# Optimization experiments

Hardware: AMD Instinct MI355X
Metric: run time of the kernel (lower is better)

The kernel has to match this reference:

```python
import jax, jax.numpy as jnp
import numpy as np

H = 8
D_MODEL = 512
D_K = D_MODEL // H


def setup_inputs() -> dict:
    key = jax.random.key(0)
    ks = jax.random.split(key, 12)
    B, S = 4, 2048
    scale = 1.0 / np.sqrt(D_MODEL)
    inp = {
        "query": jax.random.normal(ks[0], (B, S, D_MODEL), jnp.float32),
        "key": jax.random.normal(ks[1], (B, S, D_MODEL), jnp.float32),
        "value": jax.random.normal(ks[2], (B, S, D_MODEL), jnp.float32),
        "mask": jnp.ones((B, 1, S), jnp.int32),
        "Wq": jax.random.normal(ks[3], (D_MODEL, D_MODEL), jnp.float32) * scale,
        "bq": jax.random.normal(ks[4], (D_MODEL,), jnp.float32) * 0.01,
        "Wk": jax.random.normal(ks[5], (D_MODEL, D_MODEL), jnp.float32) * scale,
        "bk": jax.random.normal(ks[6], (D_MODEL,), jnp.float32) * 0.01,
        "Wv": jax.random.normal(ks[7], (D_MODEL, D_MODEL), jnp.float32) * scale,
        "bv": jax.random.normal(ks[8], (D_MODEL,), jnp.float32) * 0.01,
        "Wo": jax.random.normal(ks[9], (D_MODEL, D_MODEL), jnp.float32) * scale,
        "bo": jax.random.normal(ks[10], (D_MODEL,), jnp.float32) * 0.01,
    }
    return inp


def reference(query, key, value, mask, Wq, bq, Wk, bk, Wv, bv, Wo, bo):
    B, S, _ = query.shape

    def proj(x, W, b):
        # [B,S,D] -> [B,H,S,d_k]
        y = jnp.einsum('bsd,ed->bse', x, W) + b  # torch Linear: x @ W.T + b
        return y.reshape(B, S, H, D_K).transpose(0, 2, 1, 3)

    q = proj(query, Wq, bq)
    k = proj(key, Wk, bk)
    v = proj(value, Wv, bv)

    scores = jnp.einsum('bhqd,bhkd->bhqk', q, k) / jnp.sqrt(jnp.float32(D_K))
    m = mask[:, None, :, :]  # [B,1,1,S]
    scores = jnp.where(m == 0, jnp.float32(-1e9), scores)
    p_attn = jax.nn.softmax(scores, axis=-1)  # dropout is identity in eval
    x = jnp.einsum('bhqk,bhkd->bhqd', p_attn, v)
    x = x.transpose(0, 2, 1, 3).reshape(B, S, D_MODEL)
    return jnp.einsum('bsd,ed->bse', x, Wo) + bo
```

## Files before the change

### kernel.cpp

```cpp
#include <hip/hip_runtime.h>
#include <hip/hip_bf16.h>

#define H 8
#define DMODEL 512
#define DK 64
#define BATCH 4
#define SEQ 2048
#define M_TOTAL (BATCH*SEQ)

typedef short bf16x8 __attribute__((ext_vector_type(8)));
typedef float f32x4 __attribute__((ext_vector_type(4)));
typedef float f32x16 __attribute__((ext_vector_type(16)));

__device__ __forceinline__ unsigned short f2bf(float f) {
    unsigned int u = __builtin_bit_cast(unsigned int, f);
    u += 0x7FFFu + ((u >> 16) & 1u);
    return (unsigned short)(u >> 16);
}

__device__ __forceinline__ unsigned int pack_bf2(float a, float b) {
    unsigned int r;
    asm("v_cvt_pk_bf16_f32 %0, %1, %2" : "=v"(r) : "v"(a), "v"(b));
    return r;
}

__device__ __forceinline__ float exp2_fast(float x) {
    float r;
    asm("v_exp_f32 %0, %1" : "=v"(r) : "v"(x));
    return r;
}

__device__ __forceinline__ f32x16 zero16() {
    f32x16 z;
    #pragma unroll
    for (int i = 0; i < 16; i++) z[i] = 0.f;
    return z;
}

__global__ __launch_bounds__(256) void gemm_qkv(
    const float* __restrict__ query, const float* __restrict__ key_,
    const float* __restrict__ value,
    const float* __restrict__ Wq, const float* __restrict__ bq,
    const float* __restrict__ Wk, const float* __restrict__ bk,
    const float* __restrict__ Wv, const float* __restrict__ bv,
    unsigned short* __restrict__ Qh, unsigned short* __restrict__ Kh,
    unsigned short* __restrict__ Vt)
{
    const int z = blockIdx.z;
    const float* A    = (z == 0) ? query : (z == 1) ? key_ : value;
    const float* W    = (z == 0) ? Wq : (z == 1) ? Wk : Wv;
    const float* bias = (z == 0) ? bq : (z == 1) ? bk : bv;
    unsigned short* out = (z == 0) ? Qh : (z == 1) ? Kh : Vt;

    const int m0 = blockIdx.x * 128;
    const int n0 = blockIdx.y * 64;
    const int tid = threadIdx.x;
    const int lane = tid & 63;
    const int w = tid >> 6;
    const int g = lane >> 4, qi = lane & 15;
    const int wm = w >> 1, wn = w & 1;

    __shared__ unsigned short Alds[128 * 40];
    __shared__ unsigned short Blds[64 * 40];

    f32x4 acc[4][2];
    #pragma unroll
    for (int i = 0; i < 4; i++)
        #pragma unroll
        for (int j = 0; j < 2; j++) acc[i][j] = f32x4{0.f, 0.f, 0.f, 0.f};

    float4 aA[4], bA[2], aB[4], bB[2];

    auto ld = [&](float4 (&ar)[4], float4 (&br)[2], int k0) {
        #pragma unroll
        for (int i = 0; i < 4; i++) { int idx = tid + i * 256;
            ar[i] = *(const float4*)(A + (size_t)(m0 + (idx >> 3)) * 512 + k0 + (idx & 7) * 4); }
        #pragma unroll
        for (int i = 0; i < 2; i++) { int idx = tid + i * 256;
            br[i] = *(const float4*)(W + (size_t)(n0 + (idx >> 3)) * 512 + k0 + (idx & 7) * 4); }
    };
    auto st = [&](float4 (&ar)[4], float4 (&br)[2]) {
        #pragma unroll
        for (int i = 0; i < 4; i++) { int idx = tid + i * 256;
            uint2 p; p.x = pack_bf2(ar[i].x, ar[i].y); p.y = pack_bf2(ar[i].z, ar[i].w);
            *(uint2*)(Alds + (idx >> 3) * 40 + (idx & 7) * 4) = p; }
        #pragma unroll
        for (int i = 0; i < 2; i++) { int idx = tid + i * 256;
            uint2 p; p.x = pack_bf2(br[i].x, br[i].y); p.y = pack_bf2(br[i].z, br[i].w);
            *(uint2*)(Blds + (idx >> 3) * 40 + (idx & 7) * 4) = p; }
    };
    auto tile = [&]() {
        bf16x8 af[4], bf[2];
        #pragma unroll
        for (int mt = 0; mt < 4; mt++)
            af[mt] = *(const bf16x8*)(Alds + (wm * 64 + mt * 16 + qi) * 40 + g * 8);
        #pragma unroll
        for (int nt = 0; nt < 2; nt++)
            bf[nt] = *(const bf16x8*)(Blds + (wn * 32 + nt * 16 + qi) * 40 + g * 8);
        #pragma unroll
        for (int mt = 0; mt < 4; mt++)
            #pragma unroll
            for (int nt = 0; nt < 2; nt++)
                acc[mt][nt] = __builtin_amdgcn_mfma_f32_16x16x32_bf16(af[mt], bf[nt], acc[mt][nt], 0, 0, 0);
    };

    ld(aA, bA, 0);
    for (int k0 = 0; k0 < 512; k0 += 64) {
        __syncthreads();
        st(aA, bA);
        ld(aB, bB, k0 + 32);
        __syncthreads();
        tile();
        __syncthreads();
        st(aB, bB);
        if (k0 + 64 < 512) ld(aA, bA, k0 + 64);
        __syncthreads();
        tile();
    }

    #pragma unroll
    for (int mt = 0; mt < 4; mt++) {
        int mbase = m0 + wm * 64 + mt * 16 + g * 4;
        #pragma unroll
        for (int nt = 0; nt < 2; nt++) {
            int n = n0 + wn * 32 + nt * 16 + qi;
            float bv = bias[n];
            int h = n >> 6, dk = n & 63;
            if (z == 2) {
                int b = mbase >> 11, s = mbase & 2047;
                uint2 pk;
                pk.x = pack_bf2(acc[mt][nt][0] + bv, acc[mt][nt][1] + bv);
                pk.y = pack_bf2(acc[mt][nt][2] + bv, acc[mt][nt][3] + bv);
                *(uint2*)(out + ((size_t)(b * H + h) * 64 + dk) * SEQ + s) = pk;
            } else {
                float sc = (z == 0) ? 0.18033688011112042f : 1.0f;
                #pragma unroll
                for (int r = 0; r < 4; r++) {
                    int m = mbase + r;
                    int b = m >> 11, s = m & 2047;
                    out[((size_t)(b * H + h) * SEQ + s) * 64 + dk] = f2bf((acc[mt][nt][r] + bv) * sc);
                }
            }
        }
    }
}

__global__ __launch_bounds__(256) void gemm_o(
    const unsigned short* __restrict__ Xa, const float* __restrict__ W,
    const float* __restrict__ bias, float* __restrict__ out)
{
    const int m0 = blockIdx.x * 128;
    const int n0 = blockIdx.y * 64;
    const int tid = threadIdx.x;
    const int lane = tid & 63;
    const int w = tid >> 6;
    const int g = lane >> 4, qi = lane & 15;
    const int wm = w >> 1, wn = w & 1;

    __shared__ unsigned short Alds[128 * 40];
    __shared__ unsigned short Blds[64 * 40];

    f32x4 acc[4][2];
    #pragma unroll
    for (int i = 0; i < 4; i++)
        #pragma unroll
        for (int j = 0; j < 2; j++) acc[i][j] = f32x4{0.f, 0.f, 0.f, 0.f};

    bf16x8 aA[2], aB[2];
    float4 bA[2], bB[2];

    auto ld = [&](bf16x8 (&ar)[2], float4 (&br)[2], int k0) {
        #pragma unroll
        for (int i = 0; i < 2; i++) { int idx = tid + i * 256;
            ar[i] = *(const bf16x8*)(Xa + (size_t)(m0 + (idx >> 2)) * 512 + k0 + (idx & 3) * 8); }
        #pragma unroll
        for (int i = 0; i < 2; i++) { int idx = tid + i * 256;
            br[i] = *(const float4*)(W + (size_t)(n0 + (idx >> 3)) * 512 + k0 + (idx & 7) * 4); }
    };
    auto st = [&](bf16x8 (&ar)[2], float4 (&br)[2]) {
        #pragma unroll
        for (int i = 0; i < 2; i++) { int idx = tid + i * 256;
            *(bf16x8*)(Alds + (idx >> 2) * 40 + (idx & 3) * 8) = ar[i]; }
        #pragma unroll
        for (int i = 0; i < 2; i++) { int idx = tid + i * 256;
            uint2 p; p.x = pack_bf2(br[i].x, br[i].y); p.y = pack_bf2(br[i].z, br[i].w);
            *(uint2*)(Blds + (idx >> 3) * 40 + (idx & 7) * 4) = p; }
    };
    auto tile = [&]() {
        bf16x8 af[4], bf[2];
        #pragma unroll
        for (int mt = 0; mt < 4; mt++)
            af[mt] = *(const bf16x8*)(Alds + (wm * 64 + mt * 16 + qi) * 40 + g * 8);
        #pragma unroll
        for (int nt = 0; nt < 2; nt++)
            bf[nt] = *(const bf16x8*)(Blds + (wn * 32 + nt * 16 + qi) * 40 + g * 8);
        #pragma unroll
        for (int mt = 0; mt < 4; mt++)
            #pragma unroll
            for (int nt = 0; nt < 2; nt++)
                acc[mt][nt] = __builtin_amdgcn_mfma_f32_16x16x32_bf16(af[mt], bf[nt], acc[mt][nt], 0, 0, 0);
    };

    ld(aA, bA, 0);
    for (int k0 = 0; k0 < 512; k0 += 64) {
        __syncthreads();
        st(aA, bA);
        ld(aB, bB, k0 + 32);
        __syncthreads();
        tile();
        __syncthreads();
        st(aB, bB);
        if (k0 + 64 < 512) ld(aA, bA, k0 + 64);
        __syncthreads();
        tile();
    }

    #pragma unroll
    for (int mt = 0; mt < 4; mt++) {
        int mbase = m0 + wm * 64 + mt * 16 + g * 4;
        #pragma unroll
        for (int nt = 0; nt < 2; nt++) {
            int n = n0 + wn * 32 + nt * 16 + qi;
            float bv = bias[n];
            #pragma unroll
            for (int r = 0; r < 4; r++)
                out[(size_t)(mbase + r) * 512 + n] = acc[mt][nt][r] + bv;
        }
    }
}

__global__ __launch_bounds__(256, 2) void attn_kernel(
    const unsigned short* __restrict__ Qh,
    const unsigned short* __restrict__ Kh,
    const unsigned short* __restrict__ Vt,
    const int* __restrict__ mask,
    unsigned short* __restrict__ Xattn)
{
    const int tid = threadIdx.x;
    const int lane = tid & 63;
    const int w = tid >> 6;
    const int c = lane & 31;
    const int hi = lane >> 5;
    const int x7 = lane & 7;

    const int bid = blockIdx.x;
    const int xcd = bid & 7;
    const int slot = bid >> 3;
    const int bh = xcd * 4 + (slot >> 4);
    const int q0 = (slot & 15) * 128;
    const int b = bh >> 3;

    __shared__ unsigned short Klds[3][64 * 64];
    __shared__ unsigned short Vlds[3][64 * 64];
    __shared__ int amflag;

    bf16x8 qfr[4];
    {
        const unsigned short* Qbase =
            Qh + ((size_t)bh * SEQ + q0 + w * 32 + c) * 64 + hi * 8;
        #pragma unroll
        for (int seg = 0; seg < 4; seg++)
            qfr[seg] = *(const bf16x8*)(Qbase + seg * 16);
    }

    f32x16 acc[2];
    acc[0] = zero16();
    acc[1] = zero16();
    float l_lane = 0.f;

    const unsigned char* Kbh = (const unsigned char*)(Kh + (size_t)bh * SEQ * 64);
    const unsigned char* Vbh = (const unsigned char*)(Vt + (size_t)bh * 64 * SEQ);
    const int* maskb = mask + b * SEQ;

    if (tid == 0) amflag = 1;
    __syncthreads();
    {
        int v = 1;
        #pragma unroll
        for (int i = 0; i < 8; i++) v &= (maskb[tid + i * 256] != 0) ? 1 : 0;
        if (__ballot(v != 0) != ~0ull && lane == 0) amflag = 0;
    }
    __syncthreads();
    const bool allmask = (amflag != 0);

    const int klane = ((lane >> 3) << 7)  + (((lane & 7) ^ (lane >> 3)) << 4);
    const int vlane = ((lane >> 3) << 12) + (((lane & 7) ^ (lane >> 3)) << 4);

    const int krow = c * 128;

    auto stage = [&](const unsigned char* ks, const unsigned char* vs, int buf) {
        unsigned char* kd = (unsigned char*)&Klds[buf][0];
        unsigned char* vd = (unsigned char*)&Vlds[buf][0];
        #pragma unroll
        for (int j = 0; j < 2; j++) {
            const int cc = w + 4 * j;
            __builtin_amdgcn_global_load_lds(
                (const __attribute__((address_space(1))) unsigned int*)(ks + cc * 1024),
                (__attribute__((address_space(3))) unsigned int*)(kd + cc * 1024), 16, 0, 0);
            __builtin_amdgcn_global_load_lds(
                (const __attribute__((address_space(1))) unsigned int*)(vs + cc * 32768),
                (__attribute__((address_space(3))) unsigned int*)(vd + cc * 1024), 16, 0, 0);
        }
    };

    auto compute = [&](int t, int buf) {
        const unsigned char* KB = (const unsigned char*)&Klds[buf][0];
        const unsigned char* VB = (const unsigned char*)&Vlds[buf][0];
        const int kv0 = t << 6;

        unsigned long long mb = ~0ull;
        if (!allmask) mb = __ballot(maskb[kv0 + lane] != 0);

        #pragma unroll
        for (int kt = 0; kt < 2; kt++) {
            f32x16 sa = zero16();
            __builtin_amdgcn_s_setprio(1);
            #pragma unroll
            for (int seg = 0; seg < 4; seg++) {
                bf16x8 kf = *(const bf16x8*)(
                    KB + kt * 4096 + krow + ((((seg << 1) | hi) ^ x7) << 4));
                sa = __builtin_amdgcn_mfma_f32_32x32x16_bf16(kf, qfr[seg], sa, 0, 0, 0);
            }
            __builtin_amdgcn_s_setprio(0);

            if (mb != ~0ull) {
                #pragma unroll
                for (int r = 0; r < 16; r++) {
                    int kvl = (r & 3) + 8 * (r >> 2) + 4 * hi + 32 * kt;
                    if (!((mb >> kvl) & 1ull)) sa[r] = -1e9f;
                }
            }

            float pe[16];
            #pragma unroll
            for (int r = 0; r < 16; r++) pe[r] = exp2_fast(sa[r]);
            l_lane += (((pe[0] + pe[1]) + (pe[2] + pe[3])) +
                       ((pe[4] + pe[5]) + (pe[6] + pe[7]))) +
                      (((pe[8] + pe[9]) + (pe[10] + pe[11])) +
                       ((pe[12] + pe[13]) + (pe[14] + pe[15])));

            unsigned int a0 = pack_bf2(pe[0],  pe[1]),  a1 = pack_bf2(pe[2],  pe[3]);
            unsigned int b0 = pack_bf2(pe[4],  pe[5]),  b1 = pack_bf2(pe[6],  pe[7]);
            unsigned int c0 = pack_bf2(pe[8],  pe[9]),  c1 = pack_bf2(pe[10], pe[11]);
            unsigned int d0 = pack_bf2(pe[12], pe[13]), d1 = pack_bf2(pe[14], pe[15]);
            asm("v_permlane32_swap_b32 %0, %1" : "+v"(a0), "+v"(b0));
            asm("v_permlane32_swap_b32 %0, %1" : "+v"(a1), "+v"(b1));
            asm("v_permlane32_swap_b32 %0, %1" : "+v"(c0), "+v"(d0));
            asm("v_permlane32_swap_b32 %0, %1" : "+v"(c1), "+v"(d1));
            uint4 u0 = {a0, a1, b0, b1};
            uint4 u1 = {c0, c1, d0, d1};
            bf16x8 pf0 = __builtin_bit_cast(bf16x8, u0);
            bf16x8 pf1 = __builtin_bit_cast(bf16x8, u1);

            __builtin_amdgcn_s_setprio(1);
            #pragma unroll
            for (int dt = 0; dt < 2; dt++) {
                bf16x8 vf0 = *(const bf16x8*)(
                    VB + dt * 4096 + krow + ((((kt << 2) | 0 | hi) ^ x7) << 4));
                acc[dt] = __builtin_amdgcn_mfma_f32_32x32x16_bf16(vf0, pf0, acc[dt], 0, 0, 0);
                bf16x8 vf1 = *(const bf16x8*)(
                    VB + dt * 4096 + krow + ((((kt << 2) | 2 | hi) ^ x7) << 4));
                acc[dt] = __builtin_amdgcn_mfma_f32_32x32x16_bf16(vf1, pf1, acc[dt], 0, 0, 0);
            }
            __builtin_amdgcn_s_setprio(0);
        }
    };

    const unsigned char* ks = Kbh + klane;
    const unsigned char* vs = Vbh + vlane;

    stage(ks, vs, 0); ks += 8192; vs += 128;
    stage(ks, vs, 1); ks += 8192; vs += 128;
    int bc = 0, bs = 2;
    #pragma unroll 1
    for (int t = 0; t < 32; ++t) {
        if (t < 31) __builtin_amdgcn_s_waitcnt(0xF74);
        else        __builtin_amdgcn_s_waitcnt(0xF70);
        __builtin_amdgcn_s_barrier();
        compute(t, bc);
        if (t + 2 < 32) {
            stage(ks, vs, bs);
            ks += 8192; vs += 128;
        }
        bc = (bc == 2) ? 0 : bc + 1;
        bs = (bs == 2) ? 0 : bs + 1;
    }

    const int h = bh & 7;
    float l = l_lane + __shfl_xor(l_lane, 32);
    const float inv = 1.0f / l;
    const int s = q0 + w * 32 + c;
    size_t base = ((size_t)b * SEQ + s) * 512 + h * 64;
    #pragma unroll
    for (int dt = 0; dt < 2; dt++) {
        #pragma unroll
        for (int rg = 0; rg < 4; rg++) {
            const int d0i = rg * 8 + hi * 4 + dt * 32;
            uint2 o;
            o.x = pack_bf2(acc[dt][4 * rg]     * inv, acc[dt][4 * rg + 1] * inv);
            o.y = pack_bf2(acc[dt][4 * rg + 2] * inv, acc[dt][4 * rg + 3] * inv);
            *(uint2*)(Xattn + base + d0i) = o;
        }
    }
}

extern "C" void kernel_launch(void* const* d_in, const int* in_sizes, int n_in,
                              void* d_out, int out_size, void* d_ws, size_t ws_size,
                              hipStream_t stream)
{
    const float* query = (const float*)d_in[0];
    const float* key_  = (const float*)d_in[1];
    const float* value = (const float*)d_in[2];
    const int*   mask  = (const int*)d_in[3];
    const float* Wq = (const float*)d_in[4];
    const float* bq = (const float*)d_in[5];
    const float* Wk = (const float*)d_in[6];
    const float* bk = (const float*)d_in[7];
    const float* Wv = (const float*)d_in[8];
    const float* bv = (const float*)d_in[9];
    const float* Wo = (const float*)d_in[10];
    const float* bo = (const float*)d_in[11];

    unsigned short* Qh = (unsigned short*)d_ws;
    unsigned short* Kh = Qh + (size_t)M_TOTAL * DMODEL;
    unsigned short* Vt = Kh + (size_t)M_TOTAL * DMODEL;
    unsigned short* Xa = Vt + (size_t)M_TOTAL * DMODEL;

    hipLaunchKernelGGL(gemm_qkv, dim3(64, 8, 3), dim3(256), 0, stream,
                       query, key_, value, Wq, bq, Wk, bk, Wv, bv, Qh, Kh, Vt);
    hipLaunchKernelGGL(attn_kernel, dim3(512), dim3(256), 0, stream, Qh, Kh, Vt, mask, Xa);
    hipLaunchKernelGGL(gemm_o, dim3(64, 8), dim3(256), 0, stream, Xa, Wo, bo, (float*)d_out);
}
```

Baseline: 89.92 us.

## Split attention KV range in two and merge partials in output GEMM

Splits each attention block's key/value sequence into two halves, doubling the grid to 1024 blocks and using two-stage instead of three-stage LDS buffering with occupancy 4. Unnormalized partial outputs and row sums are written separately, and the output projection GEMM sums the two partials and divides by the combined sum while loading A. This relies on no running max being tracked, so unnormalized exponentials can be added directly. It aims to raise occupancy and parallelism on the many CUs, at the cost of extra workspace traffic and a heavier A-load in gemm_o.

```diff
diff --git a/kernel.cpp b/kernel.cpp
--- a/kernel.cpp
+++ b/kernel.cpp
@@ -28,6 +28,10 @@
     float r;
     asm("v_exp_f32 %0, %1" : "=v"(r) : "v"(x));
     return r;
+}
+
+__device__ __forceinline__ float bf2f(short v) {
+    return __builtin_bit_cast(float, ((unsigned int)(unsigned short)v) << 16);
 }
 
 __device__ __forceinline__ f32x16 zero16() {
@@ -146,7 +150,9 @@
 }
 
 __global__ __launch_bounds__(256) void gemm_o(
-    const unsigned short* __restrict__ Xa, const float* __restrict__ W,
+    const unsigned short* __restrict__ U0, const unsigned short* __restrict__ U1,
+    const float* __restrict__ lsum,
+    const float* __restrict__ W,
     const float* __restrict__ bias, float* __restrict__ out)
 {
     const int m0 = blockIdx.x * 128;
@@ -170,9 +176,27 @@
     float4 bA[2], bB[2];
 
     auto ld = [&](bf16x8 (&ar)[2], float4 (&br)[2], int k0) {
-        #pragma unroll
-        for (int i = 0; i < 2; i++) { int idx = tid + i * 256;
-            ar[i] = *(const bf16x8*)(Xa + (size_t)(m0 + (idx >> 2)) * 512 + k0 + (idx & 3) * 8); }
+        const int h = k0 >> 6;
+        #pragma unroll
+        for (int i = 0; i < 2; i++) {
+            int idx = tid + i * 256;
+            int m = m0 + (idx >> 2);
+            size_t off = (size_t)m * 512 + k0 + (idx & 3) * 8;
+            bf16x8 u0 = *(const bf16x8*)(U0 + off);
+            bf16x8 u1 = *(const bf16x8*)(U1 + off);
+            int lidx = (((m >> 11) * 8 + h) << 11) + (m & 2047);
+            float inv = 1.0f / (lsum[lidx] + lsum[65536 + lidx]);
+            uint4 p;
+            p.x = pack_bf2((bf2f(u0[0]) + bf2f(u1[0])) * inv,
+                           (bf2f(u0[1]) + bf2f(u1[1])) * inv);
+            p.y = pack_bf2((bf2f(u0[2]) + bf2f(u1[2])) * inv,
+                           (bf2f(u0[3]) + bf2f(u1[3])) * inv);
+            p.z = pack_bf2((bf2f(u0[4]) + bf2f(u1[4])) * inv,
+                           (bf2f(u0[5]) + bf2f(u1[5])) * inv);
+            p.w = pack_bf2((bf2f(u0[6]) + bf2f(u1[6])) * inv,
+                           (bf2f(u0[7]) + bf2f(u1[7])) * inv);
+            ar[i] = __builtin_bit_cast(bf16x8, p);
+        }
         #pragma unroll
         for (int i = 0; i < 2; i++) { int idx = tid + i * 256;
             br[i] = *(const float4*)(W + (size_t)(n0 + (idx >> 3)) * 512 + k0 + (idx & 7) * 4); }
@@ -229,12 +253,14 @@
     }
 }
 
-__global__ __launch_bounds__(256, 2) void attn_kernel(
+__global__ __launch_bounds__(256, 4) void attn_kernel(
     const unsigned short* __restrict__ Qh,
     const unsigned short* __restrict__ Kh,
     const unsigned short* __restrict__ Vt,
     const int* __restrict__ mask,
-    unsigned short* __restrict__ Xattn)
+    unsigned short* __restrict__ Xa0,
+    unsigned short* __restrict__ Xa1,
+    float* __restrict__ lsum)
 {
     const int tid = threadIdx.x;
     const int lane = tid & 63;
@@ -246,12 +272,14 @@
     const int bid = blockIdx.x;
     const int xcd = bid & 7;
     const int slot = bid >> 3;
-    const int bh = xcd * 4 + (slot >> 4);
-    const int q0 = (slot & 15) * 128;
+    const int bh = xcd * 4 + (slot >> 5);
+    const int rem = slot & 31;
+    const int q0 = (rem >> 1) * 128;
+    const int half = rem & 1;
     const int b = bh >> 3;
 
-    __shared__ unsigned short Klds[3][64 * 64];
-    __shared__ unsigned short Vlds[3][64 * 64];
+    __shared__ unsigned short Klds[2][64 * 64];
+    __shared__ unsigned short Vlds[2][64 * 64];
     __shared__ int amflag;
 
     bf16x8 qfr[4];
@@ -306,7 +334,7 @@
     auto compute = [&](int t, int buf) {
         const unsigned char* KB = (const unsigned char*)&Klds[buf][0];
         const unsigned char* VB = (const unsigned char*)&Vlds[buf][0];
-        const int kv0 = t << 6;
+        const int kv0 = (half << 10) + (t << 6);
 
         unsigned long long mb = ~0ull;
         if (!allmask) mb = __ballot(maskb[kv0 + lane] != 0);
@@ -366,30 +394,25 @@
         }
     };
 
-    const unsigned char* ks = Kbh + klane;
-    const unsigned char* vs = Vbh + vlane;
+    const unsigned char* ks = Kbh + ((size_t)half << 17) + klane;
+    const unsigned char* vs = Vbh + (half << 11) + vlane;
 
     stage(ks, vs, 0); ks += 8192; vs += 128;
-    stage(ks, vs, 1); ks += 8192; vs += 128;
-    int bc = 0, bs = 2;
     #pragma unroll 1
-    for (int t = 0; t < 32; ++t) {
-        if (t < 31) __builtin_amdgcn_s_waitcnt(0xF74);
-        else        __builtin_amdgcn_s_waitcnt(0xF70);
+    for (int t = 0; t < 16; ++t) {
+        __builtin_amdgcn_s_waitcnt(0xF70);
         __builtin_amdgcn_s_barrier();
-        compute(t, bc);
-        if (t + 2 < 32) {
-            stage(ks, vs, bs);
+        if (t + 1 < 16) {
+            stage(ks, vs, (t + 1) & 1);
             ks += 8192; vs += 128;
         }
-        bc = (bc == 2) ? 0 : bc + 1;
-        bs = (bs == 2) ? 0 : bs + 1;
+        compute(t, t & 1);
     }
 
     const int h = bh & 7;
     float l = l_lane + __shfl_xor(l_lane, 32);
-    const float inv = 1.0f / l;
     const int s = q0 + w * 32 + c;
+    unsigned short* Xh = half ? Xa1 : Xa0;
     size_t base = ((size_t)b * SEQ + s) * 512 + h * 64;
     #pragma unroll
     for (int dt = 0; dt < 2; dt++) {
@@ -397,11 +420,12 @@
         for (int rg = 0; rg < 4; rg++) {
             const int d0i = rg * 8 + hi * 4 + dt * 32;
             uint2 o;
-            o.x = pack_bf2(acc[dt][4 * rg]     * inv, acc[dt][4 * rg + 1] * inv);
-            o.y = pack_bf2(acc[dt][4 * rg + 2] * inv, acc[dt][4 * rg + 3] * inv);
-            *(uint2*)(Xattn + base + d0i) = o;
-        }
-    }
+            o.x = pack_bf2(acc[dt][4 * rg],     acc[dt][4 * rg + 1]);
+            o.y = pack_bf2(acc[dt][4 * rg + 2], acc[dt][4 * rg + 3]);
+            *(uint2*)(Xh + base + d0i) = o;
+        }
+    }
+    if (hi == 0) lsum[(half << 16) + (bh << 11) + s] = l;
 }
 
 extern "C" void kernel_launch(void* const* d_in, const int* in_sizes, int n_in,
@@ -421,13 +445,17 @@
     const float* Wo = (const float*)d_in[10];
     const float* bo = (const float*)d_in[11];
 
-    unsigned short* Qh = (unsigned short*)d_ws;
-    unsigned short* Kh = Qh + (size_t)M_TOTAL * DMODEL;
-    unsigned short* Vt = Kh + (size_t)M_TOTAL * DMODEL;
-    unsigned short* Xa = Vt + (size_t)M_TOTAL * DMODEL;
+    unsigned short* Qh  = (unsigned short*)d_ws;
+    unsigned short* Kh  = Qh  + (size_t)M_TOTAL * DMODEL;
+    unsigned short* Vt  = Kh  + (size_t)M_TOTAL * DMODEL;
+    unsigned short* Xa0 = Vt  + (size_t)M_TOTAL * DMODEL;
+    unsigned short* Xa1 = Xa0 + (size_t)M_TOTAL * DMODEL;
+    float* lsum = (float*)(Xa1 + (size_t)M_TOTAL * DMODEL);
 
     hipLaunchKernelGGL(gemm_qkv, dim3(64, 8, 3), dim3(256), 0, stream,
                        query, key_, value, Wq, bq, Wk, bk, Wv, bv, Qh, Kh, Vt);
-    hipLaunchKernelGGL(attn_kernel, dim3(512), dim3(256), 0, stream, Qh, Kh, Vt, mask, Xa);
-    hipLaunchKernelGGL(gemm_o, dim3(64, 8), dim3(256), 0, stream, Xa, Wo, bo, (float*)d_out);
-}
+    hipLaunchKernelGGL(attn_kernel, dim3(1024), dim3(256), 0, stream,
+                       Qh, Kh, Vt, mask, Xa0, Xa1, lsum);
+    hipLaunchKernelGGL(gemm_o, dim3(64, 8), dim3(256), 0, stream,
+                       Xa0, Xa1, lsum, Wo, bo, (float*)d_out);
+}
```

After: 106.2 us. 18.1% more time.

## Split KV tile across wave pairs, each wave handling two Q fragments

Applied to the files above, without the earlier changes.

Each wave now owns 64 query rows (two 32-row fragments) but only half of every 64-key tile. This lets each K and V fragment read from LDS feed two MFMAs, halving LDS read traffic per MFMA. The two partial outputs and row sums are combined at the end through LDS, then normalized and stored. Costs are more accumulator registers (four f32x16 plus two Q fragment sets), an extra reduction phase with barriers, and idle waves during the final store.

```diff
diff --git a/kernel.cpp b/kernel.cpp
--- a/kernel.cpp
+++ b/kernel.cpp
@@ -239,6 +239,8 @@
     const int tid = threadIdx.x;
     const int lane = tid & 63;
     const int w = tid >> 6;
+    const int ktw = w & 1;
+    const int qh = w >> 1;
     const int c = lane & 31;
     const int hi = lane >> 5;
     const int x7 = lane & 7;
@@ -254,19 +256,20 @@
     __shared__ unsigned short Vlds[3][64 * 64];
     __shared__ int amflag;
 
-    bf16x8 qfr[4];
-    {
+    bf16x8 qfr[2][4];
+    #pragma unroll
+    for (int f = 0; f < 2; f++) {
         const unsigned short* Qbase =
-            Qh + ((size_t)bh * SEQ + q0 + w * 32 + c) * 64 + hi * 8;
+            Qh + ((size_t)bh * SEQ + q0 + qh * 64 + f * 32 + c) * 64 + hi * 8;
         #pragma unroll
         for (int seg = 0; seg < 4; seg++)
-            qfr[seg] = *(const bf16x8*)(Qbase + seg * 16);
-    }
-
-    f32x16 acc[2];
-    acc[0] = zero16();
-    acc[1] = zero16();
-    float l_lane = 0.f;
+            qfr[f][seg] = *(const bf16x8*)(Qbase + seg * 16);
+    }
+
+    f32x16 acc[2][2];
+    acc[0][0] = zero16(); acc[0][1] = zero16();
+    acc[1][0] = zero16(); acc[1][1] = zero16();
+    float l_lane[2] = {0.f, 0.f};
 
     const unsigned char* Kbh = (const unsigned char*)(Kh + (size_t)bh * SEQ * 64);
     const unsigned char* Vbh = (const unsigned char*)(Vt + (size_t)bh * 64 * SEQ);
@@ -311,34 +314,36 @@
         unsigned long long mb = ~0ull;
         if (!allmask) mb = __ballot(maskb[kv0 + lane] != 0);
 
-        #pragma unroll
-        for (int kt = 0; kt < 2; kt++) {
-            f32x16 sa = zero16();
-            __builtin_amdgcn_s_setprio(1);
-            #pragma unroll
-            for (int seg = 0; seg < 4; seg++) {
-                bf16x8 kf = *(const bf16x8*)(
-                    KB + kt * 4096 + krow + ((((seg << 1) | hi) ^ x7) << 4));
-                sa = __builtin_amdgcn_mfma_f32_32x32x16_bf16(kf, qfr[seg], sa, 0, 0, 0);
+        f32x16 sa0 = zero16(), sa1 = zero16();
+        __builtin_amdgcn_s_setprio(1);
+        #pragma unroll
+        for (int seg = 0; seg < 4; seg++) {
+            bf16x8 kf = *(const bf16x8*)(
+                KB + ktw * 4096 + krow + ((((seg << 1) | hi) ^ x7) << 4));
+            sa0 = __builtin_amdgcn_mfma_f32_32x32x16_bf16(kf, qfr[0][seg], sa0, 0, 0, 0);
+            sa1 = __builtin_amdgcn_mfma_f32_32x32x16_bf16(kf, qfr[1][seg], sa1, 0, 0, 0);
+        }
+        __builtin_amdgcn_s_setprio(0);
+
+        if (mb != ~0ull) {
+            #pragma unroll
+            for (int r = 0; r < 16; r++) {
+                int kvl = (r & 3) + 8 * (r >> 2) + 4 * hi + 32 * ktw;
+                if (!((mb >> kvl) & 1ull)) { sa0[r] = -1e9f; sa1[r] = -1e9f; }
             }
-            __builtin_amdgcn_s_setprio(0);
-
-            if (mb != ~0ull) {
-                #pragma unroll
-                for (int r = 0; r < 16; r++) {
-                    int kvl = (r & 3) + 8 * (r >> 2) + 4 * hi + 32 * kt;
-                    if (!((mb >> kvl) & 1ull)) sa[r] = -1e9f;
-                }
-            }
-
+        }
+
+        bf16x8 pf[2][2];
+        #pragma unroll
+        for (int f = 0; f < 2; f++) {
+            const f32x16& sa = f ? sa1 : sa0;
             float pe[16];
             #pragma unroll
             for (int r = 0; r < 16; r++) pe[r] = exp2_fast(sa[r]);
-            l_lane += (((pe[0] + pe[1]) + (pe[2] + pe[3])) +
-                       ((pe[4] + pe[5]) + (pe[6] + pe[7]))) +
-                      (((pe[8] + pe[9]) + (pe[10] + pe[11])) +
-                       ((pe[12] + pe[13]) + (pe[14] + pe[15])));
-
+            l_lane[f] += (((pe[0] + pe[1]) + (pe[2] + pe[3])) +
+                          ((pe[4] + pe[5]) + (pe[6] + pe[7]))) +
+                         (((pe[8] + pe[9]) + (pe[10] + pe[11])) +
+                          ((pe[12] + pe[13]) + (pe[14] + pe[15])));
             unsigned int a0 = pack_bf2(pe[0],  pe[1]),  a1 = pack_bf2(pe[2],  pe[3]);
             unsigned int b0 = pack_bf2(pe[4],  pe[5]),  b1 = pack_bf2(pe[6],  pe[7]);
             unsigned int c0 = pack_bf2(pe[8],  pe[9]),  c1 = pack_bf2(pe[10], pe[11]);
@@ -349,21 +354,23 @@
             asm("v_permlane32_swap_b32 %0, %1" : "+v"(c1), "+v"(d1));
             uint4 u0 = {a0, a1, b0, b1};
             uint4 u1 = {c0, c1, d0, d1};
-            bf16x8 pf0 = __builtin_bit_cast(bf16x8, u0);
-            bf16x8 pf1 = __builtin_bit_cast(bf16x8, u1);
-
-            __builtin_amdgcn_s_setprio(1);
-            #pragma unroll
-            for (int dt = 0; dt < 2; dt++) {
-                bf16x8 vf0 = *(const bf16x8*)(
-                    VB + dt * 4096 + krow + ((((kt << 2) | 0 | hi) ^ x7) << 4));
-                acc[dt] = __builtin_amdgcn_mfma_f32_32x32x16_bf16(vf0, pf0, acc[dt], 0, 0, 0);
-                bf16x8 vf1 = *(const bf16x8*)(
-                    VB + dt * 4096 + krow + ((((kt << 2) | 2 | hi) ^ x7) << 4));
-                acc[dt] = __builtin_amdgcn_mfma_f32_32x32x16_bf16(vf1, pf1, acc[dt], 0, 0, 0);
-            }
-            __builtin_amdgcn_s_setprio(0);
-        }
+            pf[f][0] = __builtin_bit_cast(bf16x8, u0);
+            pf[f][1] = __builtin_bit_cast(bf16x8, u1);
+        }
+
+        __builtin_amdgcn_s_setprio(1);
+        #pragma unroll
+        for (int dt = 0; dt < 2; dt++) {
+            bf16x8 vf0 = *(const bf16x8*)(
+                VB + dt * 4096 + krow + ((((ktw << 2) | 0 | hi) ^ x7) << 4));
+            acc[0][dt] = __builtin_amdgcn_mfma_f32_32x32x16_bf16(vf0, pf[0][0], acc[0][dt], 0, 0, 0);
+            acc[1][dt] = __builtin_amdgcn_mfma_f32_32x32x16_bf16(vf0, pf[1][0], acc[1][dt], 0, 0, 0);
+            bf16x8 vf1 = *(const bf16x8*)(
+                VB + dt * 4096 + krow + ((((ktw << 2) | 2 | hi) ^ x7) << 4));
+            acc[0][dt] = __builtin_amdgcn_mfma_f32_32x32x16_bf16(vf1, pf[0][1], acc[0][dt], 0, 0, 0);
+            acc[1][dt] = __builtin_amdgcn_mfma_f32_32x32x16_bf16(vf1, pf[1][1], acc[1][dt], 0, 0, 0);
+        }
+        __builtin_amdgcn_s_setprio(0);
     };
 
     const unsigned char* ks = Kbh + klane;
@@ -386,20 +393,62 @@
         bs = (bs == 2) ? 0 : bs + 1;
     }
 
-    const int h = bh & 7;
-    float l = l_lane + __shfl_xor(l_lane, 32);
-    const float inv = 1.0f / l;
-    const int s = q0 + w * 32 + c;
-    size_t base = ((size_t)b * SEQ + s) * 512 + h * 64;
-    #pragma unroll
-    for (int dt = 0; dt < 2; dt++) {
-        #pragma unroll
-        for (int rg = 0; rg < 4; rg++) {
-            const int d0i = rg * 8 + hi * 4 + dt * 32;
-            uint2 o;
-            o.x = pack_bf2(acc[dt][4 * rg]     * inv, acc[dt][4 * rg + 1] * inv);
-            o.y = pack_bf2(acc[dt][4 * rg + 2] * inv, acc[dt][4 * rg + 3] * inv);
-            *(uint2*)(Xattn + base + d0i) = o;
+    float l2[2];
+    #pragma unroll
+    for (int f = 0; f < 2; f++) l2[f] = l_lane[f] + __shfl_xor(l_lane[f], 32);
+
+    __syncthreads();
+    float* abuf = (qh == 0) ? (float*)&Klds[0][0] : (float*)&Vlds[0][0];
+    float* lb = (float*)((unsigned char*)&Vlds[0][0] + 20480);
+    if (ktw == 1) {
+        float* dst = abuf + lane * 68;
+        #pragma unroll
+        for (int f = 0; f < 2; f++)
+            #pragma unroll
+            for (int dt = 0; dt < 2; dt++)
+                #pragma unroll
+                for (int rg = 0; rg < 4; rg++) {
+                    f32x4 tv = {acc[f][dt][4 * rg],     acc[f][dt][4 * rg + 1],
+                                acc[f][dt][4 * rg + 2], acc[f][dt][4 * rg + 3]};
+                    *(f32x4*)(dst + (f * 2 + dt) * 16 + rg * 4) = tv;
+                }
+        if (hi == 0) {
+            lb[qh * 64 + c]      = l2[0];
+            lb[qh * 64 + 32 + c] = l2[1];
+        }
+    }
+    __syncthreads();
+    if (ktw == 0) {
+        const float* src = abuf + lane * 68;
+        #pragma unroll
+        for (int f = 0; f < 2; f++)
+            #pragma unroll
+            for (int dt = 0; dt < 2; dt++)
+                #pragma unroll
+                for (int rg = 0; rg < 4; rg++) {
+                    f32x4 tv = *(const f32x4*)(src + (f * 2 + dt) * 16 + rg * 4);
+                    acc[f][dt][4 * rg]     += tv[0];
+                    acc[f][dt][4 * rg + 1] += tv[1];
+                    acc[f][dt][4 * rg + 2] += tv[2];
+                    acc[f][dt][4 * rg + 3] += tv[3];
+                }
+        const int h = bh & 7;
+        #pragma unroll
+        for (int f = 0; f < 2; f++) {
+            float inv = 1.0f / (l2[f] + lb[qh * 64 + f * 32 + c]);
+            const int s = q0 + qh * 64 + f * 32 + c;
+            size_t base = ((size_t)b * SEQ + s) * 512 + h * 64;
+            #pragma unroll
+            for (int dt = 0; dt < 2; dt++) {
+                #pragma unroll
+                for (int rg = 0; rg < 4; rg++) {
+                    const int d0i = rg * 8 + hi * 4 + dt * 32;
+                    uint2 o;
+                    o.x = pack_bf2(acc[f][dt][4 * rg]     * inv, acc[f][dt][4 * rg + 1] * inv);
+                    o.y = pack_bf2(acc[f][dt][4 * rg + 2] * inv, acc[f][dt][4 * rg + 3] * inv);
+                    *(uint2*)(Xattn + base + d0i) = o;
+                }
+            }
         }
     }
 }
```

After: 88.88 us (median of 2 runs). No clear change (-1.2%).
